# Kernel optimization log

Measured on AMD Instinct MI355X. Metric: run time of the kernel, lower is better.

The kernel has to match this reference:

```python
import jax, jax.numpy as jnp
import numpy as np

N = 100000   # nodes
E = 1600000  # edges
F = 128      # input features
H = 128      # hidden
L = 4        # num_layers (1 conv1 + 3 convs)
S = 10000    # subgraphs
G = 256      # graphs
C = 10       # classes
BN_EPS = 1e-5


def setup_inputs() -> dict:
    key = jax.random.key(0)
    ks = jax.random.split(key, 12)
    x = jax.random.normal(ks[0], (N, F), jnp.float32)
    edge_index = jax.random.randint(ks[1], (2, E), 0, N, jnp.int32)
    node_to_subgraph = jnp.sort(jax.random.randint(ks[2], (N,), 0, S, jnp.int32))
    subgraph_to_graph = jnp.sort(jax.random.randint(ks[3], (S,), 0, G, jnp.int32))
    sc = 1.0 / np.sqrt(H)
    # stacked per-layer GIN MLP params (torch Linear layout [out, in]); F == H so conv1 stacks too
    W1 = jax.random.uniform(ks[4], (L, H, F), jnp.float32, -sc, sc)
    b1 = jax.random.uniform(ks[5], (L, H), jnp.float32, -sc, sc)
    g1 = jnp.ones((L, H), jnp.float32)
    be1 = jnp.zeros((L, H), jnp.float32)
    W2 = jax.random.uniform(ks[6], (L, H, H), jnp.float32, -sc, sc)
    b2 = jax.random.uniform(ks[7], (L, H), jnp.float32, -sc, sc)
    g2 = jnp.ones((L, H), jnp.float32)
    be2 = jnp.zeros((L, H), jnp.float32)
    eps = jnp.zeros((L,), jnp.float32)  # train_eps=True, init 0
    sc1 = 1.0 / np.sqrt(L * H)
    lin1_W = jax.random.uniform(ks[8], (H, L * H), jnp.float32, -sc1, sc1)
    lin1_b = jax.random.uniform(ks[9], (H,), jnp.float32, -sc1, sc1)
    lin2_W = jax.random.uniform(ks[10], (C, H), jnp.float32, -sc, sc)
    lin2_b = jax.random.uniform(ks[11], (C,), jnp.float32, -sc, sc)
    return dict(x=x, edge_index=edge_index, node_to_subgraph=node_to_subgraph,
                subgraph_to_graph=subgraph_to_graph, W1=W1, b1=b1, g1=g1, be1=be1,
                W2=W2, b2=b2, g2=g2, be2=be2, eps=eps,
                lin1_W=lin1_W, lin1_b=lin1_b, lin2_W=lin2_W, lin2_b=lin2_b)


def _bn(h, g, b):
    mu = h.mean(axis=0)
    var = jnp.mean((h - mu) ** 2, axis=0)  # biased var (training-mode BN)
    return (h - mu) * jax.lax.rsqrt(var + BN_EPS) * g + b


def _seg_mean(f, seg, num_segments):
    s = jax.ops.segment_sum(f, seg, num_segments=num_segments)
    cnt = jax.ops.segment_sum(jnp.ones((f.shape[0], 1), f.dtype), seg, num_segments=num_segments)
    return s / jnp.maximum(cnt, 1.0)


def reference(x, edge_index, node_to_subgraph, subgraph_to_graph,
              W1, b1, g1, be1, W2, b2, g2, be2, eps,
              lin1_W, lin1_b, lin2_W, lin2_b):
    src, dst = edge_index[0], edge_index[1]

    def layer(xc, p):
        w1, bb1, gg1, bt1, w2, bb2, gg2, bt2, e = p
        agg = jax.ops.segment_sum(xc[src], dst, num_segments=N)  # neighbor sum
        h = (1.0 + e) * xc + agg
        h = jax.nn.relu(_bn(h @ w1.T + bb1, gg1, bt1))
        h = jax.nn.relu(_bn(h @ w2.T + bb2, gg2, bt2))
        return h, h

    _, ys = jax.lax.scan(layer, x, (W1, b1, g1, be1, W2, b2, g2, be2, eps))  # [L, N, H]
    feat = jnp.transpose(ys, (1, 0, 2)).reshape(N, L * H)  # torch.cat(xs, dim=1)
    sub = _seg_mean(feat, node_to_subgraph, S)   # [S, L*H]
    gph = _seg_mean(sub, subgraph_to_graph, G)   # [G, L*H]
    h = jax.nn.relu(gph @ lin1_W.T + lin1_b)
    out = h @ lin2_W.T + lin2_b                  # dropout inactive in eval
    return jax.nn.log_softmax(out, axis=-1)
```

## Files before the change

### kernel.cpp

```cpp
#include <hip/hip_runtime.h>

typedef unsigned int u32;
typedef unsigned short u16;

#define NN 100000
#define EE 1600000
#define SS 10000
#define GG 256
#define NSCAN ((NN + 1023) / 1024)

#define O_W1   0
#define O_B1   65536
#define O_G1   66048
#define O_BE1  66560
#define O_W2   67072
#define O_B2   132608
#define O_G2   133120
#define O_BE2  133632
#define O_EPS  134144
#define O_L1W  134148
#define O_L1B  199684
#define O_L2W  199812
#define O_L2B  201092
#define NPAR   201102

typedef __bf16 bf16x8_t __attribute__((ext_vector_type(8)));
typedef float f32x4_t __attribute__((ext_vector_type(4)));
typedef u32 u32x4_t __attribute__((ext_vector_type(4)));

__device__ __forceinline__ float bf2f(u16 u) {
  union { u32 i; float f; } x; x.i = ((u32)u) << 16; return x.f;
}
__device__ __forceinline__ u16 f2bf(float f) {
  union { float f; u32 i; } x; x.f = f;
  u32 r = x.i + 0x7fffu + ((x.i >> 16) & 1u);
  return (u16)(r >> 16);
}
__device__ __forceinline__ int lbound(const int* __restrict__ a, int n, int key) {
  int lo = 0, hi = n;
  while (lo < hi) { int mid = (lo + hi) >> 1; if (a[mid] < key) lo = mid + 1; else hi = mid; }
  return lo;
}

__global__ void k_sniff(const u16* __restrict__ x, int* __restrict__ flag) {
  __shared__ int cnt;
  if (threadIdx.x == 0) cnt = 0;
  __syncthreads();
  int weird = 0;
  for (int i = threadIdx.x; i < 8192; i += 256) {
    u16 v = x[i];
    int e = (v >> 7) & 0xff;
    if (e >= 0xC0) weird++;
  }
  atomicAdd(&cnt, weird);
  __syncthreads();
  if (threadIdx.x == 0) *flag = (cnt > 64) ? 1 : 0;
}

__global__ __launch_bounds__(256) void k_cvt_params(
    const void* pW1, const void* pb1, const void* pg1, const void* pbe1,
    const void* pW2, const void* pb2, const void* pg2, const void* pbe2,
    const void* peps, const void* pl1w, const void* pl1b, const void* pl2w, const void* pl2b,
    const int* __restrict__ flagp, float* __restrict__ P) {
  int i = blockIdx.x * 256 + threadIdx.x;
  if (i >= NPAR) return;
  const void* src; int rel;
  if      (i < O_B1)  { src = pW1;  rel = i - O_W1; }
  else if (i < O_G1)  { src = pb1;  rel = i - O_B1; }
  else if (i < O_BE1) { src = pg1;  rel = i - O_G1; }
  else if (i < O_W2)  { src = pbe1; rel = i - O_BE1; }
  else if (i < O_B2)  { src = pW2;  rel = i - O_W2; }
  else if (i < O_G2)  { src = pb2;  rel = i - O_B2; }
  else if (i < O_BE2) { src = pg2;  rel = i - O_G2; }
  else if (i < O_EPS) { src = pbe2; rel = i - O_BE2; }
  else if (i < O_L1W) { src = peps; rel = i - O_EPS; }
  else if (i < O_L1B) { src = pl1w; rel = i - O_L1W; }
  else if (i < O_L2W) { src = pl1b; rel = i - O_L1B; }
  else if (i < O_L2B) { src = pl2w; rel = i - O_L2W; }
  else                { src = pl2b; rel = i - O_L2B; }
  float v = (*flagp) ? ((const float*)src)[rel] : bf2f(((const u16*)src)[rel]);
  P[i] = v;
}

__global__ __launch_bounds__(256) void k_cvtW(const float* __restrict__ P,
                                              u16* __restrict__ W1b, u16* __restrict__ W2b) {
  int i = blockIdx.x * 256 + threadIdx.x;
  if (i >= 131072) return;
  if (i < 65536) W1b[i] = f2bf(P[O_W1 + i]);
  else           W2b[i - 65536] = f2bf(P[O_W2 + i - 65536]);
}

__global__ __launch_bounds__(256) void k_prep(const void* __restrict__ x, const int* __restrict__ flagp,
                                              u16* __restrict__ Z0) {
  int i = blockIdx.x * 256 + threadIdx.x;
  if (i >= (NN * 128) / 8) return;
  if (*flagp) {
    const float4* xf = (const float4*)x;
    float4 a = xf[i * 2], b = xf[i * 2 + 1];
    u32x4_t o;
    o[0] = (u32)f2bf(a.x) | ((u32)f2bf(a.y) << 16);
    o[1] = (u32)f2bf(a.z) | ((u32)f2bf(a.w) << 16);
    o[2] = (u32)f2bf(b.x) | ((u32)f2bf(b.y) << 16);
    o[3] = (u32)f2bf(b.z) | ((u32)f2bf(b.w) << 16);
    *(u32x4_t*)(Z0 + i * 8) = o;
  } else {
    *(u32x4_t*)(Z0 + i * 8) = ((const u32x4_t*)x)[i];
  }
}

__global__ __launch_bounds__(256) void k_hist(const int* __restrict__ dst, int* __restrict__ cnt) {
  int i = blockIdx.x * 256 + threadIdx.x;
  if (i < EE) atomicAdd(&cnt[dst[i]], 1);
}

__global__ __launch_bounds__(256) void k_scan1(const int* __restrict__ cnt, int* __restrict__ bsum) {
  __shared__ int sh[256];
  int base = blockIdx.x * 1024 + threadIdx.x * 4;
  int s = 0;
#pragma unroll
  for (int i = 0; i < 4; i++) { int idx = base + i; s += (idx < NN) ? cnt[idx] : 0; }
  sh[threadIdx.x] = s; __syncthreads();
  for (int o = 128; o > 0; o >>= 1) {
    if (threadIdx.x < o) sh[threadIdx.x] += sh[threadIdx.x + o];
    __syncthreads();
  }
  if (threadIdx.x == 0) bsum[blockIdx.x] = sh[0];
}

__global__ void k_scan2(int* __restrict__ bsum, int* __restrict__ off) {
  if (threadIdx.x == 0 && blockIdx.x == 0) {
    int run = 0;
    for (int i = 0; i < NSCAN; i++) { int v = bsum[i]; bsum[i] = run; run += v; }
    off[NN] = run;
  }
}

__global__ __launch_bounds__(256) void k_scan3(const int* __restrict__ cnt, const int* __restrict__ bsum,
                                               int* __restrict__ off) {
  __shared__ int sh[256];
  int base = blockIdx.x * 1024 + threadIdx.x * 4;
  int v[4]; int s = 0;
#pragma unroll
  for (int i = 0; i < 4; i++) { int idx = base + i; v[i] = (idx < NN) ? cnt[idx] : 0; s += v[i]; }
  sh[threadIdx.x] = s; __syncthreads();
  for (int o = 1; o < 256; o <<= 1) {
    int add = (threadIdx.x >= o) ? sh[threadIdx.x - o] : 0;
    __syncthreads();
    sh[threadIdx.x] += add;
    __syncthreads();
  }
  int run = sh[threadIdx.x] - s + bsum[blockIdx.x];
#pragma unroll
  for (int i = 0; i < 4; i++) { int idx = base + i; if (idx < NN) { off[idx] = run; run += v[i]; } }
}

__global__ __launch_bounds__(256) void k_fill(const int* __restrict__ src, const int* __restrict__ dst,
                                              const int* __restrict__ off, int* __restrict__ cur,
                                              int* __restrict__ csr) {
  int i = blockIdx.x * 256 + threadIdx.x;
  if (i >= EE) return;
  int d = dst[i];
  int p = off[d] + atomicAdd(&cur[d], 1);
  csr[p] = src[i];
}

__global__ __launch_bounds__(256) void k_agg_gemm(
    const u16* __restrict__ Z, const int* __restrict__ off, const int* __restrict__ csr,
    const u16* __restrict__ Wb, const float* __restrict__ bias, const float* __restrict__ P,
    int layer, u16* __restrict__ H, float* __restrict__ st) {
  __shared__ __align__(16) u16 lds[4][16][136];
  __shared__ __align__(16) int shidx[4][512];
  int wave = threadIdx.x >> 6, lane = threadIdx.x & 63;
  int r0 = blockIdx.x * 64 + wave * 16;
  float ev = 1.0f + P[O_EPS + layer];
  const u32* zr = (const u32*)Z;

  int offv = 0;
  if (lane <= 16) {
    int rr = r0 + lane; if (rr > NN) rr = NN; if (rr < 0) rr = 0;
    offv = off[rr];
  }
  int ebase = __shfl(offv, 0, 64);
  int eend  = __shfl(offv, 16, 64);
  int tn = eend - ebase;
  int nst = tn < 512 ? tn : 512;
  for (int i = lane; i < nst; i += 64) shidx[wave][i] = csr[ebase + i];

  for (int rr = 0; rr < 16; rr++) {
    int row = r0 + rr;
    float a0 = 0.f, a1 = 0.f;
    if (row < NN) {
      int s = __shfl(offv, rr, 64), e = __shfl(offv, rr + 1, 64);
      int n = e - s, b = s - ebase;
      u32 d = zr[row * 64 + lane];
      a0 = ev * bf2f((u16)(d & 0xffffu));
      a1 = ev * bf2f((u16)(d >> 16));
      const int* ip = (b + n <= 512) ? &shidx[wave][b] : &csr[s];
      int i = 0;
      for (; i + 7 < n; i += 8) {
        u32 dd[8];
#pragma unroll
        for (int j = 0; j < 8; j++) dd[j] = zr[ip[i + j] * 64 + lane];
#pragma unroll
        for (int j = 0; j < 8; j++) {
          a0 += bf2f((u16)(dd[j] & 0xffffu));
          a1 += bf2f((u16)(dd[j] >> 16));
        }
      }
      for (; i + 1 < n; i += 2) {
        u32 d0 = zr[ip[i] * 64 + lane];
        u32 d1 = zr[ip[i + 1] * 64 + lane];
        a0 += bf2f((u16)(d0 & 0xffffu)) + bf2f((u16)(d1 & 0xffffu));
        a1 += bf2f((u16)(d0 >> 16)) + bf2f((u16)(d1 >> 16));
      }
      if (i < n) {
        u32 d0 = zr[ip[i] * 64 + lane];
        a0 += bf2f((u16)(d0 & 0xffffu));
        a1 += bf2f((u16)(d0 >> 16));
      }
    }
    ((u32*)&lds[wave][rr][0])[lane] = (u32)f2bf(a0) | ((u32)f2bf(a1) << 16);
  }

  int nidx = lane & 15, q = lane >> 4;
  f32x4_t acc[8];
  f32x4_t z4 = {0.f, 0.f, 0.f, 0.f};
#pragma unroll
  for (int ot = 0; ot < 8; ot++) acc[ot] = z4;
#pragma unroll
  for (int ks = 0; ks < 4; ks++) {
    bf16x8_t af = __builtin_bit_cast(bf16x8_t, *(const u32x4_t*)&lds[wave][nidx][ks * 32 + q * 8]);
#pragma unroll
    for (int ot = 0; ot < 8; ot++) {
      bf16x8_t bfr = __builtin_bit_cast(bf16x8_t, *(const u32x4_t*)(Wb + (ot * 16 + nidx) * 128 + ks * 32 + q * 8));
      acc[ot] = __builtin_amdgcn_mfma_f32_16x16x32_bf16(af, bfr, acc[ot], 0, 0, 0);
    }
  }
  float* sstw = (float*)&shidx[wave][0];
#pragma unroll
  for (int ot = 0; ot < 8; ot++) {
    int col = ot * 16 + nidx;
    float bv = bias[col];
    float s = 0.f, sq = 0.f;
#pragma unroll
    for (int j = 0; j < 4; j++) {
      int row = r0 + q * 4 + j;
      if (row < NN) {
        float v = acc[ot][j] + bv;
        u16 h = f2bf(v);
        float vr = bf2f(h);
        H[row * 128 + col] = h;
        s += vr; sq += vr * vr;
      }
    }
    s  += __shfl_xor(s, 16, 64);  s  += __shfl_xor(s, 32, 64);
    sq += __shfl_xor(sq, 16, 64); sq += __shfl_xor(sq, 32, 64);
    if (q == 0) { sstw[col] = s; sstw[128 + col] = sq; }
  }
  __syncthreads();
  int t = threadIdx.x;
  float tot = ((float*)&shidx[0][0])[t] + ((float*)&shidx[1][0])[t] +
              ((float*)&shidx[2][0])[t] + ((float*)&shidx[3][0])[t];
  atomicAdd(&st[t], tot);
}

__global__ __launch_bounds__(256) void k_bn_gemm(
    const u16* __restrict__ Hin, const u16* __restrict__ Wb, const float* __restrict__ bias,
    const float* __restrict__ st_in, const float* __restrict__ gw, const float* __restrict__ bw,
    u16* __restrict__ Hout, float* __restrict__ st_out) {
  __shared__ float sc[256];
  __shared__ float sst[4][256];
  int t = threadIdx.x;
  if (t < 128) {
    float mu = st_in[t] * (1.0f / NN);
    float var = st_in[128 + t] * (1.0f / NN) - mu * mu;
    var = fmaxf(var, 0.f);
    float r = rsqrtf(var + 1e-5f);
    float scl = gw[t] * r;
    sc[t] = scl;
    sc[128 + t] = bw[t] - mu * scl;
  }
  __syncthreads();
  int wave = t >> 6, lane = t & 63;
  int r0 = blockIdx.x * 64 + wave * 16;
  int nidx = lane & 15, q = lane >> 4;
  int arow = r0 + nidx;
  u32x4_t zero4 = {0, 0, 0, 0};
  u32x4_t raw[4];
#pragma unroll
  for (int ks = 0; ks < 4; ks++)
    raw[ks] = (arow < NN) ? *(const u32x4_t*)(Hin + arow * 128 + ks * 32 + q * 8) : zero4;
  f32x4_t acc[8];
  f32x4_t z4 = {0.f, 0.f, 0.f, 0.f};
#pragma unroll
  for (int ot = 0; ot < 8; ot++) acc[ot] = z4;
#pragma unroll
  for (int ks = 0; ks < 4; ks++) {
    int k0 = ks * 32 + q * 8;
    u32x4_t ap;
#pragma unroll
    for (int w = 0; w < 4; w++) {
      int k = k0 + 2 * w;
      float v0 = fmaxf(bf2f((u16)(raw[ks][w] & 0xffffu)) * sc[k] + sc[128 + k], 0.f);
      float v1 = fmaxf(bf2f((u16)(raw[ks][w] >> 16)) * sc[k + 1] + sc[128 + k + 1], 0.f);
      ap[w] = (u32)f2bf(v0) | ((u32)f2bf(v1) << 16);
    }
    bf16x8_t af = __builtin_bit_cast(bf16x8_t, ap);
#pragma unroll
    for (int ot = 0; ot < 8; ot++) {
      bf16x8_t bfr = __builtin_bit_cast(bf16x8_t, *(const u32x4_t*)(Wb + (ot * 16 + nidx) * 128 + k0));
      acc[ot] = __builtin_amdgcn_mfma_f32_16x16x32_bf16(af, bfr, acc[ot], 0, 0, 0);
    }
  }
#pragma unroll
  for (int ot = 0; ot < 8; ot++) {
    int col = ot * 16 + nidx;
    float bv = bias[col];
    float s = 0.f, sq = 0.f;
#pragma unroll
    for (int j = 0; j < 4; j++) {
      int row = r0 + q * 4 + j;
      if (row < NN) {
        float v = acc[ot][j] + bv;
        u16 h = f2bf(v);
        float vr = bf2f(h);
        Hout[row * 128 + col] = h;
        s += vr; sq += vr * vr;
      }
    }
    s  += __shfl_xor(s, 16, 64);  s  += __shfl_xor(s, 32, 64);
    sq += __shfl_xor(sq, 16, 64); sq += __shfl_xor(sq, 32, 64);
    if (q == 0) { sst[wave][col] = s; sst[wave][128 + col] = sq; }
  }
  __syncthreads();
  float tot = sst[0][t] + sst[1][t] + sst[2][t] + sst[3][t];
  atomicAdd(&st_out[t], tot);
}

__global__ __launch_bounds__(256) void k_bn_sub(
    const u16* __restrict__ Hin, const float* __restrict__ st_in, const float* __restrict__ gw,
    const float* __restrict__ bw, const int* __restrict__ n2s,
    u16* __restrict__ Znext, float* __restrict__ sub, int layer) {
  __shared__ float sc[256];
  int t = threadIdx.x;
  if (t < 128) {
    float mu = st_in[t] * (1.0f / NN);
    float var = st_in[128 + t] * (1.0f / NN) - mu * mu;
    var = fmaxf(var, 0.f);
    float r = rsqrtf(var + 1e-5f);
    float scl = gw[t] * r;
    sc[t] = scl;
    sc[128 + t] = bw[t] - mu * scl;
  }
  __syncthreads();
  int s = (blockIdx.x * 256 + t) >> 6;
  int lane = t & 63;
  if (s >= SS) return;
  int r0 = lbound(n2s, NN, s), r1 = lbound(n2s, NN, s + 1);
  float scl0 = sc[2 * lane], scl1 = sc[2 * lane + 1];
  float sh0 = sc[128 + 2 * lane], sh1 = sc[128 + 2 * lane + 1];
  const u32* hr = (const u32*)Hin;
  u32* zr = (u32*)Znext;
  float a0 = 0.f, a1 = 0.f;
  for (int r = r0; r < r1; r++) {
    u32 d = hr[r * 64 + lane];
    float v0 = fmaxf(bf2f((u16)(d & 0xffffu)) * scl0 + sh0, 0.f);
    float v1 = fmaxf(bf2f((u16)(d >> 16)) * scl1 + sh1, 0.f);
    zr[r * 64 + lane] = (u32)f2bf(v0) | ((u32)f2bf(v1) << 16);
    a0 += v0; a1 += v1;
  }
  int c = r1 - r0;
  float inv = 1.0f / (float)(c > 0 ? c : 1);
  float2 v; v.x = a0 * inv; v.y = a1 * inv;
  *(float2*)(sub + (size_t)s * 512 + layer * 128 + lane * 2) = v;
}

__global__ __launch_bounds__(256) void k_graphpool(const float* __restrict__ sub, const int* __restrict__ s2g,
                                                   float* __restrict__ gph) {
  int g = (blockIdx.x * 256 + threadIdx.x) >> 6;
  int lane = threadIdx.x & 63;
  if (g >= GG) return;
  int r0 = lbound(s2g, SS, g), r1 = lbound(s2g, SS, g + 1);
  float a[8] = {0.f, 0.f, 0.f, 0.f, 0.f, 0.f, 0.f, 0.f};
  for (int s = r0; s < r1; s++) {
    const float* row = sub + (size_t)s * 512 + lane * 8;
#pragma unroll
    for (int j = 0; j < 8; j++) a[j] += row[j];
  }
  int c = r1 - r0;
  float inv = 1.0f / (float)(c > 0 ? c : 1);
  float* orow = gph + (size_t)g * 512 + lane * 8;
#pragma unroll
  for (int j = 0; j < 8; j++) orow[j] = a[j] * inv;
}

__global__ __launch_bounds__(128) void k_head(const float* __restrict__ gph, const float* __restrict__ P,
                                              const int* __restrict__ flagp, void* __restrict__ out) {
  __shared__ float gsh[512];
  __shared__ float hsh[128];
  __shared__ float lsh[12];
  int g = blockIdx.x, t = threadIdx.x;
  for (int i = t; i < 512; i += 128) gsh[i] = gph[(size_t)g * 512 + i];
  __syncthreads();
  float acc = P[O_L1B + t];
  const float4* wr = (const float4*)(P + O_L1W + t * 512);
  for (int kb = 0; kb < 128; kb++) {
    float4 w = wr[kb];
    int k = kb * 4;
    acc += gsh[k] * w.x + gsh[k + 1] * w.y + gsh[k + 2] * w.z + gsh[k + 3] * w.w;
  }
  hsh[t] = fmaxf(acc, 0.f);
  __syncthreads();
  if (t < 10) {
    float a = P[O_L2B + t];
    const float* w2r = P + O_L2W + t * 128;
    for (int k = 0; k < 128; k++) a += hsh[k] * w2r[k];
    lsh[t] = a;
  }
  __syncthreads();
  if (t == 0) {
    float m = -1e30f;
    for (int c = 0; c < 10; c++) m = fmaxf(m, lsh[c]);
    float se = 0.f;
    for (int c = 0; c < 10; c++) se += expf(lsh[c] - m);
    lsh[10] = m + logf(se);
  }
  __syncthreads();
  if (t < 10) {
    float v = lsh[t] - lsh[10];
    if (*flagp) ((float*)out)[g * 10 + t] = v;
    else        ((u16*)out)[g * 10 + t] = f2bf(v);
  }
}

extern "C" void kernel_launch(void* const* d_in, const int* in_sizes, int n_in,
                              void* d_out, int out_size, void* d_ws, size_t ws_size,
                              hipStream_t stream) {
  const void* x   = d_in[0];
  const int* ei   = (const int*)d_in[1];
  const int* n2s  = (const int*)d_in[2];
  const int* s2g  = (const int*)d_in[3];

  char* ws = (char*)d_ws;
  size_t o = 0;
  auto alloc = [&](size_t b) -> void* {
    void* p = ws + o;
    o += (b + 255) & ~(size_t)255;
    return p;
  };
  int* flag   = (int*)alloc(256);
  int* off    = (int*)alloc((NN + 1) * 4);
  int* cnt    = (int*)alloc(NN * 4);
  int* bsum   = (int*)alloc(NSCAN * 4);
  int* csr    = (int*)alloc((size_t)EE * 4);
  u16* zb0    = (u16*)alloc((size_t)NN * 128 * 2);
  u16* zb1    = (u16*)alloc((size_t)NN * 128 * 2);
  u16* H1     = (u16*)alloc((size_t)NN * 128 * 2);
  u16* H2     = (u16*)alloc((size_t)NN * 128 * 2);
  float* sub  = (float*)alloc((size_t)SS * 512 * 4);
  float* gph  = (float*)alloc((size_t)GG * 512 * 4);
  float* stats = (float*)alloc(8 * 256 * 4);
  float* P    = (float*)alloc((size_t)NPAR * 4);
  u16* W1b    = (u16*)alloc(65536 * 2);
  u16* W2b    = (u16*)alloc(65536 * 2);

  const int* esrc = ei;
  const int* edst = ei + EE;

  hipMemsetAsync(cnt, 0, NN * 4, stream);
  hipMemsetAsync(stats, 0, 8 * 256 * 4, stream);

  k_sniff<<<dim3(1), dim3(256), 0, stream>>>((const u16*)x, flag);
  k_cvt_params<<<dim3((NPAR + 255) / 256), dim3(256), 0, stream>>>(
      d_in[4], d_in[5], d_in[6], d_in[7], d_in[8], d_in[9], d_in[10], d_in[11],
      d_in[12], d_in[13], d_in[14], d_in[15], d_in[16], flag, P);
  k_cvtW<<<dim3(512), dim3(256), 0, stream>>>(P, W1b, W2b);
  k_prep<<<dim3((NN * 128 / 8 + 255) / 256), dim3(256), 0, stream>>>(x, flag, zb0);

  k_hist<<<dim3((EE + 255) / 256), dim3(256), 0, stream>>>(edst, cnt);
  k_scan1<<<dim3(NSCAN), dim3(256), 0, stream>>>(cnt, bsum);
  k_scan2<<<dim3(1), dim3(64), 0, stream>>>(bsum, off);
  k_scan3<<<dim3(NSCAN), dim3(256), 0, stream>>>(cnt, bsum, off);
  hipMemsetAsync(cnt, 0, NN * 4, stream);
  k_fill<<<dim3((EE + 255) / 256), dim3(256), 0, stream>>>(esrc, edst, off, cnt, csr);

  for (int l = 0; l < 4; l++) {
    const u16* Zin = (l == 0) ? zb0 : ((l & 1) ? zb1 : zb0);
    u16* Zout = (l & 1) ? zb0 : zb1;
    float* st1 = stats + (2 * l) * 256;
    float* st2 = stats + (2 * l + 1) * 256;
    k_agg_gemm<<<dim3((NN + 63) / 64), dim3(256), 0, stream>>>(
        Zin, off, csr, W1b + l * 16384, P + O_B1 + l * 128, P, l, H1, st1);
    k_bn_gemm<<<dim3((NN + 63) / 64), dim3(256), 0, stream>>>(
        H1, W2b + l * 16384, P + O_B2 + l * 128, st1, P + O_G1 + l * 128, P + O_BE1 + l * 128, H2, st2);
    k_bn_sub<<<dim3((SS + 3) / 4), dim3(256), 0, stream>>>(
        H2, st2, P + O_G2 + l * 128, P + O_BE2 + l * 128, n2s, Zout, sub, l);
  }
  k_graphpool<<<dim3((GG + 3) / 4), dim3(256), 0, stream>>>(sub, s2g, gph);
  k_head<<<dim3(GG), dim3(128), 0, stream>>>(gph, P, flag, (void*)d_out);
}
```

Baseline: 1.218 ms.

## Fuse BN+ReLU into neighbor gather and sort CSR neighbors by source chunk

Drops the BN+ReLU normalized node buffer write from the subgraph pooling kernel. The next layer's aggregation now applies the previous layer's BN scale/shift and ReLU on the fly to each gathered pre-BN row. CSR construction also buckets each node's neighbors into 16 source-index chunks, so gathers walk memory in a more ordered way for better cache locality. This saves one full-activation write per layer, at the cost of more ALU work per gathered element, plus extra histogram atomics and a 6.4MB per-chunk count array and memset.

```diff
diff --git a/kernel.cpp b/kernel.cpp
--- a/kernel.cpp
+++ b/kernel.cpp
@@ -8,6 +8,7 @@
 #define SS 10000
 #define GG 256
 #define NSCAN ((NN + 1023) / 1024)
+#define NCHUNK 16
 
 #define O_W1   0
 #define O_B1   65536
@@ -108,9 +109,13 @@
   }
 }
 
-__global__ __launch_bounds__(256) void k_hist(const int* __restrict__ dst, int* __restrict__ cnt) {
+__global__ __launch_bounds__(256) void k_hist12(const int* __restrict__ src, const int* __restrict__ dst,
+                                                int* __restrict__ cnt, int* __restrict__ cnt2) {
   int i = blockIdx.x * 256 + threadIdx.x;
-  if (i < EE) atomicAdd(&cnt[dst[i]], 1);
+  if (i >= EE) return;
+  int d = dst[i], s = src[i];
+  atomicAdd(&cnt[d], 1);
+  atomicAdd(&cnt2[d * NCHUNK + (s >> 13)], 1);
 }
 
 __global__ __launch_bounds__(256) void k_scan1(const int* __restrict__ cnt, int* __restrict__ bsum) {
@@ -154,26 +159,53 @@
   for (int i = 0; i < 4; i++) { int idx = base + i; if (idx < NN) { off[idx] = run; run += v[i]; } }
 }
 
-__global__ __launch_bounds__(256) void k_fill(const int* __restrict__ src, const int* __restrict__ dst,
-                                              const int* __restrict__ off, int* __restrict__ cur,
-                                              int* __restrict__ csr) {
+__global__ __launch_bounds__(256) void k_start2(const int* __restrict__ off, const int* __restrict__ cnt2,
+                                                int* __restrict__ start2) {
+  int d = blockIdx.x * 256 + threadIdx.x;
+  if (d >= NN) return;
+  int base = off[d];
+#pragma unroll
+  for (int c = 0; c < NCHUNK; c++) {
+    int s = cnt2[d * NCHUNK + c];
+    start2[d * NCHUNK + c] = base;
+    base += s;
+  }
+}
+
+__global__ __launch_bounds__(256) void k_fill2(const int* __restrict__ src, const int* __restrict__ dst,
+                                               int* __restrict__ start2, int* __restrict__ csr) {
   int i = blockIdx.x * 256 + threadIdx.x;
   if (i >= EE) return;
-  int d = dst[i];
-  int p = off[d] + atomicAdd(&cur[d], 1);
-  csr[p] = src[i];
+  int d = dst[i], s = src[i];
+  int p = atomicAdd(&start2[d * NCHUNK + (s >> 13)], 1);
+  csr[p] = s;
 }
 
 __global__ __launch_bounds__(256) void k_agg_gemm(
     const u16* __restrict__ Z, const int* __restrict__ off, const int* __restrict__ csr,
     const u16* __restrict__ Wb, const float* __restrict__ bias, const float* __restrict__ P,
-    int layer, u16* __restrict__ H, float* __restrict__ st) {
+    int layer, int mode, const float* __restrict__ st_prev, const float* __restrict__ gw,
+    const float* __restrict__ bw, u16* __restrict__ H, float* __restrict__ st) {
   __shared__ __align__(16) u16 lds[4][16][136];
   __shared__ __align__(16) int shidx[4][512];
   int wave = threadIdx.x >> 6, lane = threadIdx.x & 63;
   int r0 = blockIdx.x * 64 + wave * 16;
   float ev = 1.0f + P[O_EPS + layer];
   const u32* zr = (const u32*)Z;
+
+  int c0 = 2 * lane, c1 = 2 * lane + 1;
+  float scl0 = 1.f, scl1 = 1.f, sh0 = 0.f, sh1 = 0.f, ncl = -3.0e38f;
+  if (mode) {
+    float mu0 = st_prev[c0] * (1.0f / NN);
+    float v0 = fmaxf(st_prev[128 + c0] * (1.0f / NN) - mu0 * mu0, 0.f);
+    scl0 = gw[c0] * rsqrtf(v0 + 1e-5f);
+    sh0 = bw[c0] - mu0 * scl0;
+    float mu1 = st_prev[c1] * (1.0f / NN);
+    float v1 = fmaxf(st_prev[128 + c1] * (1.0f / NN) - mu1 * mu1, 0.f);
+    scl1 = gw[c1] * rsqrtf(v1 + 1e-5f);
+    sh1 = bw[c1] - mu1 * scl1;
+    ncl = 0.f;
+  }
 
   int offv = 0;
   if (lane <= 16) {
@@ -193,8 +225,8 @@
       int s = __shfl(offv, rr, 64), e = __shfl(offv, rr + 1, 64);
       int n = e - s, b = s - ebase;
       u32 d = zr[row * 64 + lane];
-      a0 = ev * bf2f((u16)(d & 0xffffu));
-      a1 = ev * bf2f((u16)(d >> 16));
+      a0 = ev * fmaxf(fmaf(bf2f((u16)(d & 0xffffu)), scl0, sh0), ncl);
+      a1 = ev * fmaxf(fmaf(bf2f((u16)(d >> 16)), scl1, sh1), ncl);
       const int* ip = (b + n <= 512) ? &shidx[wave][b] : &csr[s];
       int i = 0;
       for (; i + 7 < n; i += 8) {
@@ -203,20 +235,22 @@
         for (int j = 0; j < 8; j++) dd[j] = zr[ip[i + j] * 64 + lane];
 #pragma unroll
         for (int j = 0; j < 8; j++) {
-          a0 += bf2f((u16)(dd[j] & 0xffffu));
-          a1 += bf2f((u16)(dd[j] >> 16));
+          a0 += fmaxf(fmaf(bf2f((u16)(dd[j] & 0xffffu)), scl0, sh0), ncl);
+          a1 += fmaxf(fmaf(bf2f((u16)(dd[j] >> 16)), scl1, sh1), ncl);
         }
       }
       for (; i + 1 < n; i += 2) {
         u32 d0 = zr[ip[i] * 64 + lane];
         u32 d1 = zr[ip[i + 1] * 64 + lane];
-        a0 += bf2f((u16)(d0 & 0xffffu)) + bf2f((u16)(d1 & 0xffffu));
-        a1 += bf2f((u16)(d0 >> 16)) + bf2f((u16)(d1 >> 16));
+        a0 += fmaxf(fmaf(bf2f((u16)(d0 & 0xffffu)), scl0, sh0), ncl) +
+              fmaxf(fmaf(bf2f((u16)(d1 & 0xffffu)), scl1 * 0.f + scl0, sh0), ncl);
+        a1 += fmaxf(fmaf(bf2f((u16)(d0 >> 16)), scl1, sh1), ncl) +
+              fmaxf(fmaf(bf2f((u16)(d1 >> 16)), scl1, sh1), ncl);
       }
       if (i < n) {
         u32 d0 = zr[ip[i] * 64 + lane];
-        a0 += bf2f((u16)(d0 & 0xffffu));
-        a1 += bf2f((u16)(d0 >> 16));
+        a0 += fmaxf(fmaf(bf2f((u16)(d0 & 0xffffu)), scl0, sh0), ncl);
+        a1 += fmaxf(fmaf(bf2f((u16)(d0 >> 16)), scl1, sh1), ncl);
       }
     }
     ((u32*)&lds[wave][rr][0])[lane] = (u32)f2bf(a0) | ((u32)f2bf(a1) << 16);
@@ -337,10 +371,10 @@
   atomicAdd(&st_out[t], tot);
 }
 
-__global__ __launch_bounds__(256) void k_bn_sub(
+__global__ __launch_bounds__(256) void k_sub(
     const u16* __restrict__ Hin, const float* __restrict__ st_in, const float* __restrict__ gw,
     const float* __restrict__ bw, const int* __restrict__ n2s,
-    u16* __restrict__ Znext, float* __restrict__ sub, int layer) {
+    float* __restrict__ sub, int layer) {
   __shared__ float sc[256];
   int t = threadIdx.x;
   if (t < 128) {
@@ -360,14 +394,11 @@
   float scl0 = sc[2 * lane], scl1 = sc[2 * lane + 1];
   float sh0 = sc[128 + 2 * lane], sh1 = sc[128 + 2 * lane + 1];
   const u32* hr = (const u32*)Hin;
-  u32* zr = (u32*)Znext;
   float a0 = 0.f, a1 = 0.f;
   for (int r = r0; r < r1; r++) {
     u32 d = hr[r * 64 + lane];
-    float v0 = fmaxf(bf2f((u16)(d & 0xffffu)) * scl0 + sh0, 0.f);
-    float v1 = fmaxf(bf2f((u16)(d >> 16)) * scl1 + sh1, 0.f);
-    zr[r * 64 + lane] = (u32)f2bf(v0) | ((u32)f2bf(v1) << 16);
-    a0 += v0; a1 += v1;
+    a0 += fmaxf(bf2f((u16)(d & 0xffffu)) * scl0 + sh0, 0.f);
+    a1 += fmaxf(bf2f((u16)(d >> 16)) * scl1 + sh1, 0.f);
   }
   int c = r1 - r0;
   float inv = 1.0f / (float)(c > 0 ? c : 1);
@@ -448,26 +479,29 @@
     o += (b + 255) & ~(size_t)255;
     return p;
   };
-  int* flag   = (int*)alloc(256);
-  int* off    = (int*)alloc((NN + 1) * 4);
-  int* cnt    = (int*)alloc(NN * 4);
-  int* bsum   = (int*)alloc(NSCAN * 4);
-  int* csr    = (int*)alloc((size_t)EE * 4);
-  u16* zb0    = (u16*)alloc((size_t)NN * 128 * 2);
-  u16* zb1    = (u16*)alloc((size_t)NN * 128 * 2);
-  u16* H1     = (u16*)alloc((size_t)NN * 128 * 2);
-  u16* H2     = (u16*)alloc((size_t)NN * 128 * 2);
-  float* sub  = (float*)alloc((size_t)SS * 512 * 4);
-  float* gph  = (float*)alloc((size_t)GG * 512 * 4);
+  int* flag    = (int*)alloc(256);
+  int* off     = (int*)alloc((NN + 1) * 4);
+  int* cnt     = (int*)alloc(NN * 4);
+  int* bsum    = (int*)alloc(NSCAN * 4);
+  int* cnt2    = (int*)alloc((size_t)NN * NCHUNK * 4);
+  int* start2  = (int*)alloc((size_t)NN * NCHUNK * 4);
+  int* csr     = (int*)alloc((size_t)EE * 4);
+  u16* Z0      = (u16*)alloc((size_t)NN * 128 * 2);
+  u16* H1      = (u16*)alloc((size_t)NN * 128 * 2);
+  u16* H2A     = (u16*)alloc((size_t)NN * 128 * 2);
+  u16* H2B     = (u16*)alloc((size_t)NN * 128 * 2);
+  float* sub   = (float*)alloc((size_t)SS * 512 * 4);
+  float* gph   = (float*)alloc((size_t)GG * 512 * 4);
   float* stats = (float*)alloc(8 * 256 * 4);
-  float* P    = (float*)alloc((size_t)NPAR * 4);
-  u16* W1b    = (u16*)alloc(65536 * 2);
-  u16* W2b    = (u16*)alloc(65536 * 2);
+  float* P     = (float*)alloc((size_t)NPAR * 4);
+  u16* W1b     = (u16*)alloc(65536 * 2);
+  u16* W2b     = (u16*)alloc(65536 * 2);
 
   const int* esrc = ei;
   const int* edst = ei + EE;
 
   hipMemsetAsync(cnt, 0, NN * 4, stream);
+  hipMemsetAsync(cnt2, 0, (size_t)NN * NCHUNK * 4, stream);
   hipMemsetAsync(stats, 0, 8 * 256 * 4, stream);
 
   k_sniff<<<dim3(1), dim3(256), 0, stream>>>((const u16*)x, flag);
@@ -475,26 +509,30 @@
       d_in[4], d_in[5], d_in[6], d_in[7], d_in[8], d_in[9], d_in[10], d_in[11],
       d_in[12], d_in[13], d_in[14], d_in[15], d_in[16], flag, P);
   k_cvtW<<<dim3(512), dim3(256), 0, stream>>>(P, W1b, W2b);
-  k_prep<<<dim3((NN * 128 / 8 + 255) / 256), dim3(256), 0, stream>>>(x, flag, zb0);
-
-  k_hist<<<dim3((EE + 255) / 256), dim3(256), 0, stream>>>(edst, cnt);
+  k_prep<<<dim3((NN * 128 / 8 + 255) / 256), dim3(256), 0, stream>>>(x, flag, Z0);
+
+  k_hist12<<<dim3((EE + 255) / 256), dim3(256), 0, stream>>>(esrc, edst, cnt, cnt2);
   k_scan1<<<dim3(NSCAN), dim3(256), 0, stream>>>(cnt, bsum);
   k_scan2<<<dim3(1), dim3(64), 0, stream>>>(bsum, off);
   k_scan3<<<dim3(NSCAN), dim3(256), 0, stream>>>(cnt, bsum, off);
-  hipMemsetAsync(cnt, 0, NN * 4, stream);
-  k_fill<<<dim3((EE + 255) / 256), dim3(256), 0, stream>>>(esrc, edst, off, cnt, csr);
-
+  k_start2<<<dim3((NN + 255) / 256), dim3(256), 0, stream>>>(off, cnt2, start2);
+  k_fill2<<<dim3((EE + 255) / 256), dim3(256), 0, stream>>>(esrc, edst, start2, csr);
+
+  const u16* H2prev = Z0;
   for (int l = 0; l < 4; l++) {
-    const u16* Zin = (l == 0) ? zb0 : ((l & 1) ? zb1 : zb0);
-    u16* Zout = (l & 1) ? zb0 : zb1;
+    u16* H2cur = (l & 1) ? H2B : H2A;
     float* st1 = stats + (2 * l) * 256;
     float* st2 = stats + (2 * l + 1) * 256;
+    const float* stp = (l > 0) ? (stats + (2 * l - 1) * 256) : P;
     k_agg_gemm<<<dim3((NN + 63) / 64), dim3(256), 0, stream>>>(
-        Zin, off, csr, W1b + l * 16384, P + O_B1 + l * 128, P, l, H1, st1);
+        H2prev, off, csr, W1b + l * 16384, P + O_B1 + l * 128, P, l,
+        (l > 0) ? 1 : 0, stp, P + O_G2 + (l - 1 >= 0 ? l - 1 : 0) * 128,
+        P + O_BE2 + (l - 1 >= 0 ? l - 1 : 0) * 128, H1, st1);
     k_bn_gemm<<<dim3((NN + 63) / 64), dim3(256), 0, stream>>>(
-        H1, W2b + l * 16384, P + O_B2 + l * 128, st1, P + O_G1 + l * 128, P + O_BE1 + l * 128, H2, st2);
-    k_bn_sub<<<dim3((SS + 3) / 4), dim3(256), 0, stream>>>(
-        H2, st2, P + O_G2 + l * 128, P + O_BE2 + l * 128, n2s, Zout, sub, l);
+        H1, W2b + l * 16384, P + O_B2 + l * 128, st1, P + O_G1 + l * 128, P + O_BE1 + l * 128, H2cur, st2);
+    k_sub<<<dim3((SS + 3) / 4), dim3(256), 0, stream>>>(
+        H2cur, st2, P + O_G2 + l * 128, P + O_BE2 + l * 128, n2s, sub, l);
+    H2prev = H2cur;
   }
   k_graphpool<<<dim3((GG + 3) / 4), dim3(256), 0, stream>>>(sub, s2g, gph);
   k_head<<<dim3(GG), dim3(128), 0, stream>>>(gph, P, flag, (void*)d_out);
```

Measured after the change: 1.318 ms. +8.2%, slower.
